# Optimization experiments

Measured on AMD Instinct MI355X. Metric: run time of the kernel, lower is better.

The kernel has to match this reference:

```python
import jax, jax.numpy as jnp
import numpy as np

DIM_CODES = 512
DICT_SIZE = 512
EMBED_DIM = 16
BATCH = 512


def setup_inputs() -> dict:
    key = jax.random.key(0)
    k1, k2 = jax.random.split(key)
    mu = jax.random.normal(k1, (BATCH, DIM_CODES * EMBED_DIM), dtype=jnp.float32)
    dictionary = jax.random.normal(k2, (DIM_CODES, DICT_SIZE, EMBED_DIM), dtype=jnp.float32)
    return {"mu": mu, "dictionary": dictionary}


def reference(mu, dictionary):
    # mu: [B, C*E], dictionary: [C, K, E]
    B = mu.shape[0]
    C, K, E = dictionary.shape
    mu3 = mu.reshape(B, C, E)
    # pairwise squared distance ||mu - d||^2 = ||mu||^2 + ||d||^2 - 2 mu.d -> [B, C, K]
    dist = (jnp.sum(mu3 * mu3, axis=-1)[..., None]
            + jnp.sum(dictionary * dictionary, axis=-1)[None]
            - 2.0 * jnp.einsum('bce,cke->bck', mu3, dictionary))
    idx = jnp.argmin(dist, axis=-1)  # [B, C] int
    # gather nearest codebook entries: per-code index into its own codebook
    z_embed = dictionary[jnp.arange(C)[None, :], idx]  # [B, C, E]
    z_embed = z_embed.reshape(B, C * E)
    # TransferGrad: forward = z_embed, backward passes grad straight-through to mu
    z = mu + jax.lax.stop_gradient(z_embed - mu)
    one_hot_idx = jax.nn.one_hot(idx, K, dtype=mu.dtype)  # [B, C, K]
    return z, z_embed, one_hot_idx
```

## Files before the change

### kernel.cpp

```cpp
#include <hip/hip_runtime.h>
#include <float.h>

constexpr int C    = 512;
constexpr int K    = 512;
constexpr int E    = 16;
constexpr int B    = 512;
constexpr int MUS  = C * E;
constexpr int R    = 4;

typedef float f32x4 __attribute__((ext_vector_type(4)));

__launch_bounds__(128, 1)
__global__ void vq_scan(const float* __restrict__ mu,
                        const float* __restrict__ dict,
                        float* __restrict__ z,
                        float* __restrict__ zq,
                        int*   __restrict__ idx_t)
{
    const int c    = blockIdx.x;
    const int tid  = threadIdx.x;
    const int lane = tid & 63;
    const int wave = tid >> 6;

    __shared__ __align__(16) float dict_s[K * E];
    __shared__ float nrm_s[K];

    const float* __restrict__ dbase = dict + (size_t)c * K * E;

#pragma unroll
    for (int rep = 0; rep < 4; ++rep) {
        const int k = tid + rep * 128;
        const float4* p = reinterpret_cast<const float4*>(dbase + k * E);
        const float4 d0 = p[0], d1 = p[1], d2 = p[2], d3 = p[3];
        float s = d0.x * d0.x;
        s = fmaf(d0.y, d0.y, s); s = fmaf(d0.z, d0.z, s); s = fmaf(d0.w, d0.w, s);
        s = fmaf(d1.x, d1.x, s); s = fmaf(d1.y, d1.y, s);
        s = fmaf(d1.z, d1.z, s); s = fmaf(d1.w, d1.w, s);
        s = fmaf(d2.x, d2.x, s); s = fmaf(d2.y, d2.y, s);
        s = fmaf(d2.z, d2.z, s); s = fmaf(d2.w, d2.w, s);
        s = fmaf(d3.x, d3.x, s); s = fmaf(d3.y, d3.y, s);
        s = fmaf(d3.z, d3.z, s); s = fmaf(d3.w, d3.w, s);
        float4* q4 = reinterpret_cast<float4*>(&dict_s[k * E]);
        q4[0] = d0; q4[1] = d1; q4[2] = d2; q4[3] = d3;
        nrm_s[k] = s;
    }
    __syncthreads();

    float4 m[R][4];
    float  nm[R];
#pragma unroll
    for (int s = 0; s < R; ++s) {
        const int b = tid + 128 * s;
        const float4* p = reinterpret_cast<const float4*>(
            mu + (size_t)b * MUS + c * E);
        m[s][0] = p[0]; m[s][1] = p[1]; m[s][2] = p[2]; m[s][3] = p[3];
        float v = m[s][0].x * m[s][0].x;
        v = fmaf(m[s][0].y, m[s][0].y, v);
        v = fmaf(m[s][0].z, m[s][0].z, v);
        v = fmaf(m[s][0].w, m[s][0].w, v);
#pragma unroll
        for (int t = 1; t < 4; ++t) {
            v = fmaf(m[s][t].x, m[s][t].x, v);
            v = fmaf(m[s][t].y, m[s][t].y, v);
            v = fmaf(m[s][t].z, m[s][t].z, v);
            v = fmaf(m[s][t].w, m[s][t].w, v);
        }
        nm[s] = v;
    }

    float bd[R], sec[R];
    int   bk[R];
#pragma unroll
    for (int s = 0; s < R; ++s) { bd[s] = FLT_MAX; sec[s] = FLT_MAX; bk[s] = K; }

    const float4* __restrict__ ds4 = reinterpret_cast<const float4*>(dict_s);
#pragma unroll 4
    for (int k = 0; k < K; ++k) {
        const float4 d0 = ds4[k * 4 + 0];
        const float4 d1 = ds4[k * 4 + 1];
        const float4 d2 = ds4[k * 4 + 2];
        const float4 d3 = ds4[k * 4 + 3];
        const float  nr = nrm_s[k];
#pragma unroll
        for (int s = 0; s < R; ++s) {
            float acc = d0.x * m[s][0].x;
            acc = fmaf(d0.y, m[s][0].y, acc);
            acc = fmaf(d0.z, m[s][0].z, acc);
            acc = fmaf(d0.w, m[s][0].w, acc);
            acc = fmaf(d1.x, m[s][1].x, acc);
            acc = fmaf(d1.y, m[s][1].y, acc);
            acc = fmaf(d1.z, m[s][1].z, acc);
            acc = fmaf(d1.w, m[s][1].w, acc);
            acc = fmaf(d2.x, m[s][2].x, acc);
            acc = fmaf(d2.y, m[s][2].y, acc);
            acc = fmaf(d2.z, m[s][2].z, acc);
            acc = fmaf(d2.w, m[s][2].w, acc);
            acc = fmaf(d3.x, m[s][3].x, acc);
            acc = fmaf(d3.y, m[s][3].y, acc);
            acc = fmaf(d3.z, m[s][3].z, acc);
            acc = fmaf(d3.w, m[s][3].w, acc);
            const float dist = fmaf(-2.0f, acc, nm[s] + nr);
            const bool  lt   = dist < bd[s];
            sec[s] = lt ? bd[s] : fminf(sec[s], dist);
            bd[s]  = lt ? dist : bd[s];
            bk[s]  = lt ? k : bk[s];
        }
    }

#pragma unroll
    for (int s = 0; s < R; ++s) {
        unsigned long long trig = __ballot(sec[s] < bd[s] + 1e-3f);
        while (trig) {
            const int r = __ffsll(trig) - 1;
            trig &= trig - 1;
            const int row = (wave << 6) + r + 128 * s;
            const float* __restrict__ qrow = mu + (size_t)row * MUS + c * E;

            double nmuD = 0.0;
#pragma unroll
            for (int t = 0; t < E; ++t) {
                const double mt = (double)qrow[t];
                nmuD += mt * mt;
            }
            double bD = DBL_MAX;
            int    bK = K;
#pragma unroll
            for (int i = 0; i < 8; ++i) {
                const int kk = lane + 64 * i;
                const float* dk = &dict_s[kk * E];
                double nd = 0.0, dt = 0.0;
#pragma unroll
                for (int t = 0; t < 4; ++t) {
                    const double dx = dk[4 * t + 0], dy = dk[4 * t + 1];
                    const double dz = dk[4 * t + 2], dw = dk[4 * t + 3];
                    const double mx = qrow[4 * t + 0], my = qrow[4 * t + 1];
                    const double mz = qrow[4 * t + 2], mw = qrow[4 * t + 3];
                    nd += dx * dx + dy * dy + dz * dz + dw * dw;
                    dt += dx * mx + dy * my + dz * mz + dw * mw;
                }
                const double dist = nmuD + nd - 2.0 * dt;
                if (dist < bD) { bD = dist; bK = kk; }
            }
#pragma unroll
            for (int off = 32; off; off >>= 1) {
                const double od = __shfl_down(bD, off);
                const int    ok = __shfl_down(bK, off);
                if (od < bD || (od == bD && ok < bK)) { bD = od; bK = ok; }
            }
            const int kwin = __shfl(bK, 0);
            if (lane == r) bk[s] = kwin;
        }
    }

#pragma unroll
    for (int s = 0; s < R; ++s) {
        const int b = tid + 128 * s;
        idx_t[c * B + b] = bk[s];

        const float4* dwin = reinterpret_cast<const float4*>(&dict_s[bk[s] * E]);
        const float4 q0 = dwin[0], q1 = dwin[1], q2 = dwin[2], q3 = dwin[3];
        float* zqp = zq + (size_t)b * MUS + (size_t)c * E;
        float* zp  = z  + (size_t)b * MUS + (size_t)c * E;
        reinterpret_cast<float4*>(zqp)[0] = q0;
        reinterpret_cast<float4*>(zqp)[1] = q1;
        reinterpret_cast<float4*>(zqp)[2] = q2;
        reinterpret_cast<float4*>(zqp)[3] = q3;
        float4 z0, z1, z2, z3;
        z0.x = m[s][0].x + (q0.x - m[s][0].x); z0.y = m[s][0].y + (q0.y - m[s][0].y);
        z0.z = m[s][0].z + (q0.z - m[s][0].z); z0.w = m[s][0].w + (q0.w - m[s][0].w);
        z1.x = m[s][1].x + (q1.x - m[s][1].x); z1.y = m[s][1].y + (q1.y - m[s][1].y);
        z1.z = m[s][1].z + (q1.z - m[s][1].z); z1.w = m[s][1].w + (q1.w - m[s][1].w);
        z2.x = m[s][2].x + (q2.x - m[s][2].x); z2.y = m[s][2].y + (q2.y - m[s][2].y);
        z2.z = m[s][2].z + (q2.z - m[s][2].z); z2.w = m[s][2].w + (q2.w - m[s][2].w);
        z3.x = m[s][3].x + (q3.x - m[s][3].x); z3.y = m[s][3].y + (q3.y - m[s][3].y);
        z3.z = m[s][3].z + (q3.z - m[s][3].z); z3.w = m[s][3].w + (q3.w - m[s][3].w);
        reinterpret_cast<float4*>(zp)[0] = z0;
        reinterpret_cast<float4*>(zp)[1] = z1;
        reinterpret_cast<float4*>(zp)[2] = z2;
        reinterpret_cast<float4*>(zp)[3] = z3;
    }
}

__launch_bounds__(256)
__global__ void vq_onehot(const int* __restrict__ idx_t,
                          float* __restrict__ oh)
{
    const long TOT = (long)B * C * K / 4;
    const long stride = (long)gridDim.x * blockDim.x;
    long f4 = (long)blockIdx.x * blockDim.x + threadIdx.x;
#pragma unroll 4
    for (; f4 < TOT; f4 += stride) {
        const int rowu = __builtin_amdgcn_readfirstlane((int)(f4 >> 7));
        const int bb   = rowu >> 9;
        const int cc   = rowu & (C - 1);
        const int kk   = idx_t[cc * B + bb];
        const int k0   = ((int)f4 & 127) << 2;
        f32x4 v;
        v.x = (k0 + 0 == kk) ? 1.0f : 0.0f;
        v.y = (k0 + 1 == kk) ? 1.0f : 0.0f;
        v.z = (k0 + 2 == kk) ? 1.0f : 0.0f;
        v.w = (k0 + 3 == kk) ? 1.0f : 0.0f;
        __builtin_nontemporal_store(v, reinterpret_cast<f32x4*>(oh) + f4);
    }
}

extern "C" void kernel_launch(void* const* d_in, const int* in_sizes, int n_in,
                              void* d_out, int out_size, void* d_ws, size_t ws_size,
                              hipStream_t stream)
{
    const float* mu   = (const float*)d_in[0];
    const float* dict = (const float*)d_in[1];

    float* z  = (float*)d_out;
    float* zq = z  + (size_t)B * C * E;
    float* oh = zq + (size_t)B * C * E;

    int* idx_t = (int*)d_ws;

    vq_scan<<<dim3(C), 128, 0, stream>>>(mu, dict, z, zq, idx_t);
    vq_onehot<<<2048, 256, 0, stream>>>(idx_t, oh);
}
```

Baseline: 669.8 us.

## Split codebook scan across waves and batch halves with shared-memory argmin merge

```diff
diff --git a/kernel.cpp b/kernel.cpp
--- a/kernel.cpp
+++ b/kernel.cpp
@@ -6,11 +6,13 @@
 constexpr int E    = 16;
 constexpr int B    = 512;
 constexpr int MUS  = C * E;
+constexpr int RB   = 256;
 constexpr int R    = 4;
+constexpr int KW   = K / 4;
 
 typedef float f32x4 __attribute__((ext_vector_type(4)));
 
-__launch_bounds__(128, 1)
+__launch_bounds__(256, 2)
 __global__ void vq_scan(const float* __restrict__ mu,
                         const float* __restrict__ dict,
                         float* __restrict__ z,
@@ -18,18 +20,22 @@
                         int*   __restrict__ idx_t)
 {
     const int c    = blockIdx.x;
+    const int b0   = blockIdx.y * RB;
     const int tid  = threadIdx.x;
     const int lane = tid & 63;
     const int wave = tid >> 6;
 
     __shared__ __align__(16) float dict_s[K * E];
     __shared__ float nrm_s[K];
+    __shared__ float bdm[4][RB];
+    __shared__ float secm[4][RB];
+    __shared__ int   bkm[4][RB];
 
     const float* __restrict__ dbase = dict + (size_t)c * K * E;
 
 #pragma unroll
-    for (int rep = 0; rep < 4; ++rep) {
-        const int k = tid + rep * 128;
+    for (int rep = 0; rep < 2; ++rep) {
+        const int k = tid + rep * 256;
         const float4* p = reinterpret_cast<const float4*>(dbase + k * E);
         const float4 d0 = p[0], d1 = p[1], d2 = p[2], d3 = p[3];
         float s = d0.x * d0.x;
@@ -50,7 +56,7 @@
     float  nm[R];
 #pragma unroll
     for (int s = 0; s < R; ++s) {
-        const int b = tid + 128 * s;
+        const int b = b0 + lane + 64 * s;
         const float4* p = reinterpret_cast<const float4*>(
             mu + (size_t)b * MUS + c * E);
         m[s][0] = p[0]; m[s][1] = p[1]; m[s][2] = p[2]; m[s][3] = p[3];
@@ -74,8 +80,10 @@
     for (int s = 0; s < R; ++s) { bd[s] = FLT_MAX; sec[s] = FLT_MAX; bk[s] = K; }
 
     const float4* __restrict__ ds4 = reinterpret_cast<const float4*>(dict_s);
+    const int kbase = wave * KW;
 #pragma unroll 4
-    for (int k = 0; k < K; ++k) {
+    for (int i = 0; i < KW; ++i) {
+        const int k = kbase + i;
         const float4 d0 = ds4[k * 4 + 0];
         const float4 d1 = ds4[k * 4 + 1];
         const float4 d2 = ds4[k * 4 + 2];
@@ -109,11 +117,30 @@
 
 #pragma unroll
     for (int s = 0; s < R; ++s) {
-        unsigned long long trig = __ballot(sec[s] < bd[s] + 1e-3f);
+        const int ell = lane + 64 * s;
+        bdm[wave][ell]  = bd[s];
+        secm[wave][ell] = sec[s];
+        bkm[wave][ell]  = bk[s];
+    }
+    __syncthreads();
+
+    float gbd = bdm[0][tid], gsec = secm[0][tid];
+    int   gbk = bkm[0][tid];
+#pragma unroll
+    for (int w = 1; w < 4; ++w) {
+        const float bw = bdm[w][tid];
+        const float sw = secm[w][tid];
+        const int   kw = bkm[w][tid];
+        if (bw < gbd) { gsec = fminf(gbd, sw); gbd = bw; gbk = kw; }
+        else          { gsec = fminf(gsec, bw); }
+    }
+
+    {
+        unsigned long long trig = __ballot(gsec < gbd + 1e-3f);
         while (trig) {
             const int r = __ffsll(trig) - 1;
             trig &= trig - 1;
-            const int row = (wave << 6) + r + 128 * s;
+            const int row = b0 + (wave << 6) + r;
             const float* __restrict__ qrow = mu + (size_t)row * MUS + c * E;
 
             double nmuD = 0.0;
@@ -127,7 +154,7 @@
 #pragma unroll
             for (int i = 0; i < 8; ++i) {
                 const int kk = lane + 64 * i;
-                const float* dk = &dict_s[kk * E];
+                const float* dk = dbase + (size_t)kk * E;
                 double nd = 0.0, dt = 0.0;
 #pragma unroll
                 for (int t = 0; t < 4; ++t) {
@@ -148,17 +175,20 @@
                 if (od < bD || (od == bD && ok < bK)) { bD = od; bK = ok; }
             }
             const int kwin = __shfl(bK, 0);
-            if (lane == r) bk[s] = kwin;
+            if (lane == r) gbk = kwin;
         }
     }
 
-#pragma unroll
-    for (int s = 0; s < R; ++s) {
-        const int b = tid + 128 * s;
-        idx_t[c * B + b] = bk[s];
-
-        const float4* dwin = reinterpret_cast<const float4*>(&dict_s[bk[s] * E]);
+    {
+        const int b = b0 + tid;
+        idx_t[c * B + b] = gbk;
+
+        const float4* mp = reinterpret_cast<const float4*>(
+            mu + (size_t)b * MUS + c * E);
+        const float4 mm0 = mp[0], mm1 = mp[1], mm2 = mp[2], mm3 = mp[3];
+        const float4* dwin = reinterpret_cast<const float4*>(&dict_s[gbk * E]);
         const float4 q0 = dwin[0], q1 = dwin[1], q2 = dwin[2], q3 = dwin[3];
+
         float* zqp = zq + (size_t)b * MUS + (size_t)c * E;
         float* zp  = z  + (size_t)b * MUS + (size_t)c * E;
         reinterpret_cast<float4*>(zqp)[0] = q0;
@@ -166,14 +196,14 @@
         reinterpret_cast<float4*>(zqp)[2] = q2;
         reinterpret_cast<float4*>(zqp)[3] = q3;
         float4 z0, z1, z2, z3;
-        z0.x = m[s][0].x + (q0.x - m[s][0].x); z0.y = m[s][0].y + (q0.y - m[s][0].y);
-        z0.z = m[s][0].z + (q0.z - m[s][0].z); z0.w = m[s][0].w + (q0.w - m[s][0].w);
-        z1.x = m[s][1].x + (q1.x - m[s][1].x); z1.y = m[s][1].y + (q1.y - m[s][1].y);
-        z1.z = m[s][1].z + (q1.z - m[s][1].z); z1.w = m[s][1].w + (q1.w - m[s][1].w);
-        z2.x = m[s][2].x + (q2.x - m[s][2].x); z2.y = m[s][2].y + (q2.y - m[s][2].y);
-        z2.z = m[s][2].z + (q2.z - m[s][2].z); z2.w = m[s][2].w + (q2.w - m[s][2].w);
-        z3.x = m[s][3].x + (q3.x - m[s][3].x); z3.y = m[s][3].y + (q3.y - m[s][3].y);
-        z3.z = m[s][3].z + (q3.z - m[s][3].z); z3.w = m[s][3].w + (q3.w - m[s][3].w);
+        z0.x = mm0.x + (q0.x - mm0.x); z0.y = mm0.y + (q0.y - mm0.y);
+        z0.z = mm0.z + (q0.z - mm0.z); z0.w = mm0.w + (q0.w - mm0.w);
+        z1.x = mm1.x + (q1.x - mm1.x); z1.y = mm1.y + (q1.y - mm1.y);
+        z1.z = mm1.z + (q1.z - mm1.z); z1.w = mm1.w + (q1.w - mm1.w);
+        z2.x = mm2.x + (q2.x - mm2.x); z2.y = mm2.y + (q2.y - mm2.y);
+        z2.z = mm2.z + (q2.z - mm2.z); z2.w = mm2.w + (q2.w - mm2.w);
+        z3.x = mm3.x + (q3.x - mm3.x); z3.y = mm3.y + (q3.y - mm3.y);
+        z3.z = mm3.z + (q3.z - mm3.z); z3.w = mm3.w + (q3.w - mm3.w);
         reinterpret_cast<float4*>(zp)[0] = z0;
         reinterpret_cast<float4*>(zp)[1] = z1;
         reinterpret_cast<float4*>(zp)[2] = z2;
@@ -217,6 +247,6 @@
 
     int* idx_t = (int*)d_ws;
 
-    vq_scan<<<dim3(C), 128, 0, stream>>>(mu, dict, z, zq, idx_t);
+    vq_scan<<<dim3(C, B / RB), 256, 0, stream>>>(mu, dict, z, zq, idx_t);
     vq_onehot<<<2048, 256, 0, stream>>>(idx_t, oh);
 }
```

New measurement: 666.1 us. About the same (-0.6%).
